# Performance work log

Measured on AMD Instinct MI355X. Metric: run time of the kernel, lower is better.

## Reference

```python
import jax, jax.numpy as jnp
import numpy as np

B, SEQ, H = 256, 200, 256
NFFT, HOP = 16, 8
FREQ = NFFT // 2 + 1          # 9
NSEG = SEQ // HOP + 1         # 26 (SEQ % HOP == 0 -> pad_len == 0)
FACTOR = 2


def _gelu(x):
    return jax.nn.gelu(x, approximate=False)  # torch nn.GELU / F.gelu default = exact erf


def _layernorm(x, w, b, eps=1e-12):
    u = x.mean(-1, keepdims=True)
    s = ((x - u) ** 2).mean(-1, keepdims=True)
    return w * (x - u) / jnp.sqrt(s + eps) + b


def _mixer(xr, xi, w1, b1, w2, b2):
    # complex MLP: einsum '...ijk,jkl->...ijl' with per-kept-dim weights
    e = lambda a, w: jnp.einsum('bijk,jkl->bijl', a, w)
    o1r = _gelu(e(xr, w1[0]) - e(xi, w1[1]) + b1[0])
    o1i = _gelu(e(xi, w1[0]) + e(xr, w1[1]) + b1[1])
    o2r = e(o1r, w2[0]) - e(o1i, w2[1]) + b2[0]
    # NOTE: faithful to the source bug: o1_image used in BOTH terms of o2_image
    o2i = e(o1i, w2[0]) + e(o1i, w2[1]) + b2[1]
    return o2r, o2i


def _stft(x):
    # torch.stft(n_fft=NFFT, hop=HOP, center=True, onesided=True, normalized=True,
    #            pad_mode='constant', window=None -> rectangular ones)
    pad = NFFT // 2
    xp = jnp.pad(x, ((0, 0), (pad, pad)))
    idx = jnp.arange(NSEG)[:, None] * HOP + jnp.arange(NFFT)[None, :]
    frames = xp[:, idx]                                    # [N, NSEG, NFFT]
    spec = jnp.fft.rfft(frames, axis=-1) * (NFFT ** -0.5)  # normalized=True
    return jnp.swapaxes(spec, -1, -2)                      # [N, FREQ, NSEG]


def _istft(spec):
    # torch.istft(center=True, normalized=True, rectangular window)
    n = spec.shape[0]
    frames = jnp.fft.irfft(jnp.swapaxes(spec, -1, -2) * (NFFT ** 0.5), n=NFFT, axis=-1)
    L = (NSEG - 1) * HOP + NFFT
    idx = (jnp.arange(NSEG)[:, None] * HOP + jnp.arange(NFFT)[None, :]).ravel()
    y = jnp.zeros((n, L), frames.dtype).at[:, idx].add(frames.reshape(n, -1))
    env = jnp.zeros((L,), frames.dtype).at[idx].add(1.0)   # window**2 overlap-add
    pad = NFFT // 2
    out_len = (NSEG - 1) * HOP                              # = SEQ
    return y[:, pad:pad + out_len] / env[pad:pad + out_len]


def setup_inputs() -> dict:
    key = jax.random.key(0)
    ks = jax.random.split(key, 24)
    p = lambda k, sh: jax.random.normal(k, sh, jnp.float32) * 0.02
    d = {}
    d["input_tensor"] = jax.random.normal(ks[0], (B, SEQ, H), jnp.float32)
    # grouped conv2d: weight [NSEG, 1, H, FREQ] -> stored as [NSEG, H, FREQ]
    d["conv_w"] = p(ks[1], (NSEG, H, FREQ)); d["conv_b"] = p(ks[2], (NSEG,))
    d["fm_w1"] = p(ks[3], (2, NSEG, FREQ, FREQ * FACTOR)); d["fm_b1"] = p(ks[4], (2, NSEG, FREQ * FACTOR))
    d["fm_w2"] = p(ks[5], (2, NSEG, FREQ * FACTOR, FREQ)); d["fm_b2"] = p(ks[6], (2, NSEG, FREQ))
    d["cm_w1"] = p(ks[7], (2, NSEG, H, H * FACTOR)); d["cm_b1"] = p(ks[8], (2, NSEG, H * FACTOR))
    d["cm_w2"] = p(ks[9], (2, NSEG, H * FACTOR, H)); d["cm_b2"] = p(ks[10], (2, NSEG, H))
    d["sm_w1"] = p(ks[11], (2, FREQ, NSEG, NSEG * FACTOR)); d["sm_b1"] = p(ks[12], (2, FREQ, NSEG * FACTOR))
    d["sm_w2"] = p(ks[13], (2, FREQ, NSEG * FACTOR, NSEG)); d["sm_b2"] = p(ks[14], (2, FREQ, NSEG))
    d["ln_w"] = jnp.ones((H,), jnp.float32); d["ln_b"] = jnp.zeros((H,), jnp.float32)
    d["ff_w1"] = p(ks[15], (H, 4 * H)); d["ff_b1"] = p(ks[16], (4 * H,))
    d["ff_w2"] = p(ks[17], (4 * H, H)); d["ff_b2"] = p(ks[18], (H,))
    d["ff_ln_w"] = jnp.ones((H,), jnp.float32); d["ff_ln_b"] = jnp.zeros((H,), jnp.float32)
    return d


def reference(input_tensor, conv_w, conv_b, fm_w1, fm_b1, fm_w2, fm_b2,
              cm_w1, cm_b1, cm_w2, cm_b2, sm_w1, sm_b1, sm_w2, sm_b2,
              ln_w, ln_b, ff_w1, ff_b1, ff_w2, ff_b2, ff_ln_w, ff_ln_b):
    b, seq, h = input_tensor.shape
    x = jnp.swapaxes(input_tensor, -1, -2).reshape(b * h, seq)  # pad_len == 0
    spec = _stft(x).reshape(b, h, FREQ, NSEG)
    xr, xi = spec.real, spec.imag
    xnorm = jnp.sqrt(xr ** 2 + xi ** 2)                         # [b,h,F,S]
    # grouped conv2d with full (H,FREQ) kernel == per-segment weighted sum
    w = jnp.einsum('bhfs,shf->bs', xnorm, conv_w) + conv_b
    w = w + jnp.exp(jnp.arange(1 - NSEG, 1, dtype=jnp.float32))  # exp decay bias
    xr = xr * w[:, None, None, :]
    xi = xi * w[:, None, None, :]
    # -> [b,h,S,F]: frequency mixing (kept=segment, mixed=freq)
    xr = jnp.swapaxes(xr, -1, -2); xi = jnp.swapaxes(xi, -1, -2)
    xr, xi = _mixer(xr, xi, fm_w1, fm_b1, fm_w2, fm_b2)
    # -> [b,F,S,h]: channel mixing (kept=segment, mixed=hidden)
    xr = jnp.swapaxes(xr, 1, 3); xi = jnp.swapaxes(xi, 1, 3)
    xr, xi = _mixer(xr, xi, cm_w1, cm_b1, cm_w2, cm_b2)
    # -> [b,h,F,S]: segment mixing (kept=freq, mixed=segment)
    xr = jnp.transpose(xr, (0, 3, 1, 2)); xi = jnp.transpose(xi, (0, 3, 1, 2))
    xr, xi = _mixer(xr, xi, sm_w1, sm_b1, sm_w2, sm_b2)
    spec = (xr + 1j * xi).reshape(b * h, FREQ, NSEG)
    y = _istft(spec)[:, :seq].reshape(b, h, seq)
    y = jnp.swapaxes(y, -1, -2)                                  # [b,seq,h]
    hs = _layernorm(y + input_tensor, ln_w, ln_b)                # dropout p=0
    ff = _gelu(hs @ ff_w1 + ff_b1) @ ff_w2 + ff_b2
    return _layernorm(ff + hs, ff_ln_w, ff_ln_b)
```

## Files before the change

kernel.cpp:

```cpp
#include <hip/hip_runtime.h>
#include <hip/hip_bf16.h>
#include <math.h>

typedef __hip_bfloat16 bf16;
typedef short bf16x8 __attribute__((ext_vector_type(8)));
typedef float f32x4 __attribute__((ext_vector_type(4)));

#define B_    256
#define SEQ_  200
#define H_    256
#define FREQ_ 9
#define NSEG_ 26
#define LDS64 64

__device__ __forceinline__ float ldb(const bf16* p, size_t i){ return __bfloat162float(p[i]); }
__device__ __forceinline__ void stb(bf16* p, size_t i, float v){ p[i] = __float2bfloat16(v); }
__device__ __forceinline__ short f2b(float v){ union{bf16 b; short s;} c; c.b = __float2bfloat16(v); return c.s; }
__device__ __forceinline__ unsigned short f2bu(float v){ union{bf16 b; unsigned short s;} c; c.b = __float2bfloat16(v); return c.s; }
__device__ __forceinline__ float gelu_(float x){
  float y  = 0.7978845608f*(x + 0.044715f*x*x*x);
  float ay = fabsf(y);
  float e  = __expf(-2.f*ay);
  float th = 1.f - 2.f*e*__builtin_amdgcn_rcpf(1.f + e);
  th = copysignf(th, y);
  return 0.5f*x*(1.f + th);
}

__device__ __constant__ float CT16[16] = {
  1.0f, 0.9238795325f, 0.7071067812f, 0.3826834324f, 0.0f, -0.3826834324f, -0.7071067812f, -0.9238795325f,
 -1.0f,-0.9238795325f,-0.7071067812f,-0.3826834324f, 0.0f,  0.3826834324f, 0.7071067812f,  0.9238795325f};
__device__ __constant__ float ST16[16] = {
  0.0f, 0.3826834324f, 0.7071067812f, 0.9238795325f, 1.0f,  0.9238795325f, 0.7071067812f,  0.3826834324f,
  0.0f,-0.3826834324f,-0.7071067812f,-0.9238795325f,-1.0f, -0.9238795325f,-0.7071067812f, -0.3826834324f};

__device__ __forceinline__ void gload16(const short* g, short* l){
  __builtin_amdgcn_global_load_lds(
      (const __attribute__((address_space(1))) unsigned int*)(const void*)g,
      (__attribute__((address_space(3))) unsigned int*)(void*)l, 16, 0, 0);
}

template<int ROWS>
__device__ __forceinline__ void stage_tile(short* lds, const short* src, int rstride, int tid){
  int rl = tid >> 3;
  int c  = tid & 7;
  #pragma unroll
  for(int p=0; p<ROWS/32; p++){
    int r = p*32 + rl;
    int csrc = c ^ (r & 7);
    gload16(src + (size_t)r*rstride + csrc*8, lds + r*LDS64 + c*8);
  }
}

__device__ __forceinline__ void mma_bk64(const short* lA, const short* lB, int wm, int wn,
                                         int lane, f32x4 acc[4][4]){
  int m_l = lane & 15, quad = lane >> 4;
  int sw = m_l & 7;
  #pragma unroll
  for(int ks=0; ks<64; ks+=32){
    int cs = (((ks>>3) + quad) ^ sw) * 8;
    bf16x8 a[4], b[4];
    #pragma unroll
    for(int i=0;i<4;i++) a[i] = *(const bf16x8*)&lA[(wm + i*16 + m_l)*LDS64 + cs];
    #pragma unroll
    for(int j=0;j<4;j++) b[j] = *(const bf16x8*)&lB[(wn + j*16 + m_l)*LDS64 + cs];
    #pragma unroll
    for(int i=0;i<4;i++)
      #pragma unroll
      for(int j=0;j<4;j++)
        acc[i][j] = __builtin_amdgcn_mfma_f32_16x16x32_bf16(a[i], b[j], acc[i][j], 0,0,0);
  }
}

__global__ __launch_bounds__(256) void k_prep_b1(const float* __restrict__ w1, short* __restrict__ B1t){
  int g = blockIdx.x;
  int jt = g & 7, ht = (g>>3)&3, p = (g>>5)&1, s = g>>6;
  __shared__ float tile[64][65];
  int t = threadIdx.x;
  const float* src = w1 + (size_t)p*3407872 + (size_t)s*131072;
  #pragma unroll
  for(int q=0;q<16;q++){
    int r = q*4 + (t>>6), c = t & 63;
    tile[r][c] = src[(size_t)(ht*64 + r)*512 + jt*64 + c];
  }
  __syncthreads();
  int n_l = t >> 2, kc = (t & 3)*16;
  short tA[16] __attribute__((aligned(16)));
  short tB[16] __attribute__((aligned(16)));
  #pragma unroll
  for(int i=0;i<16;i++){
    float v = tile[kc+i][n_l];
    tA[i] = (p==0) ? f2b(v) : f2b(-v);
    tB[i] = f2b(v);
  }
  int j = jt*64 + n_l, h = ht*64 + kc;
  size_t d1, d2;
  if(p==0){ d1 = ((size_t)(s*1024 + j))*512 + h;
            d2 = ((size_t)(s*1024 + 512 + j))*512 + 256 + h; }
  else    { d1 = ((size_t)(s*1024 + j))*512 + 256 + h;
            d2 = ((size_t)(s*1024 + 512 + j))*512 + h; }
  *(int4*)&B1t[d1] = *(int4*)&tA[0]; *(int4*)&B1t[d1+8] = *(int4*)&tA[8];
  *(int4*)&B1t[d2] = *(int4*)&tB[0]; *(int4*)&B1t[d2+8] = *(int4*)&tB[8];
}

__global__ __launch_bounds__(256) void k_prep_b2(const float* __restrict__ w2,
                                                 short* __restrict__ B2r, short* __restrict__ B2i){
  int g = blockIdx.x;
  int ht = g & 3, jt = (g>>2)&7, s = g>>5;
  __shared__ float t0[64][65], t1[64][65];
  int t = threadIdx.x;
  const float* s0 = w2 + (size_t)s*131072;
  const float* s1 = w2 + 3407872 + (size_t)s*131072;
  #pragma unroll
  for(int q=0;q<16;q++){
    int r = q*4 + (t>>6), c = t & 63;
    t0[r][c] = s0[(size_t)(jt*64 + r)*256 + ht*64 + c];
    t1[r][c] = s1[(size_t)(jt*64 + r)*256 + ht*64 + c];
  }
  __syncthreads();
  int n_l = t >> 2, jc = (t & 3)*16;
  short ta[16] __attribute__((aligned(16)));
  short tb[16] __attribute__((aligned(16)));
  short tc[16] __attribute__((aligned(16)));
  #pragma unroll
  for(int i=0;i<16;i++){
    float v0 = t0[jc+i][n_l], v1 = t1[jc+i][n_l];
    ta[i] = f2b(v0); tb[i] = f2b(-v1); tc[i] = f2b(v0+v1);
  }
  int n = ht*64 + n_l, j = jt*64 + jc;
  size_t dr = ((size_t)(s*256 + n))*1024 + j;
  size_t di = ((size_t)(s*256 + n))*512 + j;
  *(int4*)&B2r[dr]     = *(int4*)&ta[0]; *(int4*)&B2r[dr+8]     = *(int4*)&ta[8];
  *(int4*)&B2r[dr+512] = *(int4*)&tb[0]; *(int4*)&B2r[dr+520]   = *(int4*)&tb[8];
  *(int4*)&B2i[di]     = *(int4*)&tc[0]; *(int4*)&B2i[di+8]     = *(int4*)&tc[8];
}

__global__ __launch_bounds__(256) void k_transp(const float* __restrict__ src, short* __restrict__ dst,
                                                int R, int C){
  int ct = blockIdx.x % (C/64);
  int rt = blockIdx.x / (C/64);
  __shared__ float tile[64][65];
  int t = threadIdx.x;
  #pragma unroll
  for(int p=0;p<16;p++){
    int r = p*4 + (t>>6), c = t & 63;
    tile[r][c] = src[(size_t)(rt*64 + r)*C + ct*64 + c];
  }
  __syncthreads();
  int row_out = t >> 2, rc = (t & 3)*16;
  short tmp[16] __attribute__((aligned(16)));
  #pragma unroll
  for(int i=0;i<16;i++) tmp[i] = f2b(tile[rc+i][row_out]);
  size_t base = (size_t)(ct*64 + row_out)*R + rt*64 + rc;
  *(int4*)&dst[base] = *(int4*)&tmp[0]; *(int4*)&dst[base+8] = *(int4*)&tmp[8];
}

__global__ __launch_bounds__(256) void k_prep_sm(const float* __restrict__ w1, const float* __restrict__ w2,
                                                 short* __restrict__ B1sm, short* __restrict__ B2sm){
  int f = blockIdx.x;
  int t = threadIdx.x;
  for(int idx=t; idx<8192; idx+=256){
    int jp = idx >> 6, k = idx & 63;
    float v = 0.f;
    if(jp < 104){
      int j = (jp < 52) ? jp : jp - 52;
      if(k < 26){
        int s = k;
        v = (jp < 52) ? w1[f*1352 + s*52 + j] : w1[12168 + f*1352 + s*52 + j];
      } else if(k >= 32 && k < 58){
        int s = k - 32;
        v = (jp < 52) ? -w1[12168 + f*1352 + s*52 + j] : w1[f*1352 + s*52 + j];
      }
    }
    B1sm[(size_t)f*8192 + idx] = f2b(v);
  }
  for(int idx=t; idx<8192; idx+=256){
    int sop = idx >> 7, k = idx & 127;
    float v = 0.f;
    if(sop < 26){
      if(k < 52)       v = w2[f*1352 + k*26 + sop];
      else if(k < 104) v = -w2[12168 + f*1352 + (k-52)*26 + sop];
    } else if(sop < 52){
      int so = sop - 26;
      if(k >= 52 && k < 104)
        v = w2[f*1352 + (k-52)*26 + so] + w2[12168 + f*1352 + (k-52)*26 + so];
    }
    B2sm[(size_t)f*8192 + idx] = f2b(v);
  }
}

__global__ __launch_bounds__(256) void k_prep_fm(const float* __restrict__ w1, const float* __restrict__ w2,
                                                 short* __restrict__ B1fm, short* __restrict__ B2fm){
  int s = blockIdx.x;
  int t = threadIdx.x;
  for(int idx=t; idx<1536; idx+=256){
    int n = idx >> 5, k = idx & 31;
    float v = 0.f;
    if(n < 18){
      if(k < 9)       v = w1[s*162 + k*18 + n];
      else if(k < 18) v = -w1[4212 + s*162 + (k-9)*18 + n];
    } else if(n < 36){
      int j = n - 18;
      if(k < 9)       v = w1[4212 + s*162 + k*18 + j];
      else if(k < 18) v = w1[s*162 + (k-9)*18 + j];
    }
    B1fm[s*1536 + idx] = f2b(v);
  }
  for(int idx=t; idx<2048; idx+=256){
    int n = idx >> 6, k = idx & 63;
    float v = 0.f;
    if(n < 9){
      if(k < 18)      v = w2[s*162 + k*9 + n];
      else if(k < 36) v = -w2[4212 + s*162 + (k-18)*9 + n];
    } else if(n < 18){
      int f = n - 9;
      if(k >= 18 && k < 36)
        v = w2[s*162 + (k-18)*9 + f] + w2[4212 + s*162 + (k-18)*9 + f];
    }
    B2fm[s*2048 + idx] = f2b(v);
  }
}

__global__ __launch_bounds__(256) void k_prep_cw(const float* __restrict__ cw, float* __restrict__ cwT){
  int s = blockIdx.x; int t = threadIdx.x;
  __shared__ float tile[2304];
  for(int i=t; i<2304; i+=256) tile[i] = cw[s*2304 + i];
  __syncthreads();
  #pragma unroll
  for(int f=0; f<9; f++) cwT[(s*9+f)*256 + t] = tile[t*9+f];
}

#define LX1 40
#define LG1 72
__global__ __launch_bounds__(256) void k_sfm2(const float* __restrict__ inp,
                                              const float* __restrict__ cwT, const float* __restrict__ cb,
                                              const short* __restrict__ B1fm, const short* __restrict__ B2fm,
                                              const float* __restrict__ bb1, const float* __restrict__ bb2,
                                              bf16* __restrict__ oR, bf16* __restrict__ oI){
  int blk = blockIdx.x; int b = blk / NSEG_; int s = blk % NSEG_; int t = threadIdx.x;
  int lane = t & 63, wave = t >> 6, m_l = lane & 15, quad = lane >> 4;
  __shared__ __align__(16) short sm[20736];
  __shared__ float red[256];
  __shared__ float lb1f[48];
  short* lX  = sm;
  short* lB1 = sm + 10240;
  short* lG  = sm;
  short* lB2 = sm + 18432;

  {
    const short* src1 = B1fm + s*1536;
    for(int idx=t; idx<768; idx+=256){
      int r = idx >> 4, c = idx & 15;
      *(unsigned*)&lB1[r*LX1 + c*2] = *(const unsigned*)&src1[r*32 + c*2];
    }
    const short* src2 = B2fm + s*2048;
    for(int idx=t; idx<1024; idx+=256){
      int r = idx >> 5, c = idx & 31;
      *(unsigned*)&lB2[r*LG1 + c*2] = *(const unsigned*)&src2[r*64 + c*2];
    }
    if(t < 48) lb1f[t] = (t < 18) ? bb1[s*18 + t] : (t < 36 ? bb1[468 + s*18 + (t-18)] : 0.f);
  }

  float cwv[9];
  #pragma unroll
  for(int f=0;f<9;f++) cwv[f] = cwT[(s*9+f)*256 + t];

  float xv[16];
  int t0 = s*8 - 8;
  #pragma unroll
  for(int k=0;k<16;k++){
    int tt = t0 + k;
    xv[k] = (tt>=0 && tt<SEQ_) ? inp[(size_t)(b*SEQ_+tt)*H_ + t] : 0.0f;
  }
  float xr[9], xi[9];
  float acc = 0.f;
  #pragma unroll
  for(int f=0;f<FREQ_;f++){
    float ar=0.f, ai=0.f;
    #pragma unroll
    for(int k=0;k<16;k++){
      int m = (f*k) & 15;
      ar += xv[k]*CT16[m];
      ai -= xv[k]*ST16[m];
    }
    xr[f] = 0.25f*ar; xi[f] = 0.25f*ai;
    acc += sqrtf(xr[f]*xr[f] + xi[f]*xi[f]) * cwv[f];
  }

  red[t] = acc; __syncthreads();
  for(int off=128; off>0; off>>=1){ if(t<off) red[t] += red[t+off]; __syncthreads(); }
  float wv = red[0] + cb[s] + __expf((float)(s - (NSEG_-1)));

  {
    float vb[32];
    #pragma unroll
    for(int f=0;f<9;f++){ vb[f] = xr[f]*wv; vb[9+f] = xi[f]*wv; }
    #pragma unroll
    for(int k=18;k<32;k++) vb[k] = 0.f;
    union { unsigned u[16]; int4 v4[4]; } pk;
    #pragma unroll
    for(int c=0;c<16;c++)
      pk.u[c] = (unsigned)f2bu(vb[2*c]) | ((unsigned)f2bu(vb[2*c+1]) << 16);
    #pragma unroll
    for(int q=0;q<4;q++) *(int4*)&lX[t*LX1 + q*8] = pk.v4[q];
  }
  __syncthreads();

  int h0 = wave*64;
  f32x4 acc1[4][3];
  #pragma unroll
  for(int i=0;i<4;i++)
    #pragma unroll
    for(int j=0;j<3;j++) acc1[i][j] = (f32x4){0.f,0.f,0.f,0.f};
  {
    bf16x8 a1[4], b1v[3];
    #pragma unroll
    for(int i=0;i<4;i++) a1[i] = *(const bf16x8*)&lX[(h0 + i*16 + m_l)*LX1 + quad*8];
    #pragma unroll
    for(int j=0;j<3;j++) b1v[j] = *(const bf16x8*)&lB1[(j*16 + m_l)*LX1 + quad*8];
    #pragma unroll
    for(int i=0;i<4;i++)
      #pragma unroll
      for(int j=0;j<3;j++)
        acc1[i][j] = __builtin_amdgcn_mfma_f32_16x16x32_bf16(a1[i], b1v[j], acc1[i][j], 0,0,0);
  }
  __syncthreads();

  #pragma unroll
  for(int i=0;i<4;i++){
    #pragma unroll
    for(int j=0;j<3;j++){
      int n = j*16 + m_l;
      float bias = lb1f[n];
      #pragma unroll
      for(int r=0;r<4;r++){
        int row = h0 + i*16 + quad*4 + r;
        lG[row*LG1 + n] = f2b(gelu_(acc1[i][j][r] + bias));
      }
    }
  }
  #pragma unroll
  for(int c=0;c<8;c++) *(unsigned*)&lG[t*LG1 + 48 + c*2] = 0u;
  __syncthreads();

  f32x4 acc2[4][2];
  #pragma unroll
  for(int i=0;i<4;i++)
    #pragma unroll
    for(int j=0;j<2;j++) acc2[i][j] = (f32x4){0.f,0.f,0.f,0.f};
  #pragma unroll
  for(int ks=0; ks<64; ks+=32){
    bf16x8 a2[4], b2v[2];
    #pragma unroll
    for(int i=0;i<4;i++) a2[i] = *(const bf16x8*)&lG[(h0 + i*16 + m_l)*LG1 + ks + quad*8];
    #pragma unroll
    for(int j=0;j<2;j++) b2v[j] = *(const bf16x8*)&lB2[(j*16 + m_l)*LG1 + ks + quad*8];
    #pragma unroll
    for(int i=0;i<4;i++)
      #pragma unroll
      for(int j=0;j<2;j++)
        acc2[i][j] = __builtin_amdgcn_mfma_f32_16x16x32_bf16(a2[i], b2v[j], acc2[i][j], 0,0,0);
  }

  #pragma unroll
  for(int j=0;j<2;j++){
    int n = j*16 + m_l;
    if(n < 18){
      bool isI = n >= 9;
      int f = isI ? n-9 : n;
      float bias = isI ? bb2[234 + s*9 + f] : bb2[s*9 + f];
      bf16* outp = isI ? oI : oR;
      size_t base = ((size_t)(s*B_ + b)*FREQ_ + f)*H_;
      #pragma unroll
      for(int i=0;i<4;i++){
        int h = h0 + i*16 + quad*4;
        short pk[4] __attribute__((aligned(8)));
        #pragma unroll
        for(int r=0;r<4;r++) pk[r] = f2b(acc2[i][j][r] + bias);
        *(int2*)&outp[base + h] = *(const int2*)&pk[0];
      }
    }
  }
}

__global__ __launch_bounds__(256) void k_cm1(const bf16* __restrict__ Xr, const bf16* __restrict__ Xi,
                                             const short* __restrict__ B1t, const float* __restrict__ b1bias,
                                             short* __restrict__ H, int half){
  int nt = blockIdx.x & 7, mt = (blockIdx.x >> 3) % 9, s = blockIdx.x / 72;
  int tid = threadIdx.x, lane = tid & 63, wave = tid >> 6;
  int wm = (wave & 1)*64, wn = (wave >> 1)*64;
  __shared__ __align__(16) short lA[128*LDS64];
  __shared__ __align__(16) short lB[128*LDS64];
  f32x4 acc[4][4];
  #pragma unroll
  for(int i=0;i<4;i++)
    #pragma unroll
    for(int j=0;j<4;j++) acc[i][j] = (f32x4){0.f,0.f,0.f,0.f};
  int rowbase = half*1152 + mt*128;
  const short* Bbase = B1t + ((size_t)(s*1024 + nt*128))*512;
  for(int k0=0; k0<512; k0+=64){
    const short* Asrc = (k0 < 256)
      ? (const short*)(Xr + ((size_t)(s*2304 + rowbase))*256 + k0)
      : (const short*)(Xi + ((size_t)(s*2304 + rowbase))*256 + (k0-256));
    stage_tile<128>(lA, Asrc, 256, tid);
    stage_tile<128>(lB, Bbase + k0, 512, tid);
    __syncthreads();
    mma_bk64(lA, lB, wm, wn, lane, acc);
    __syncthreads();
  }
  int m_l = lane & 15, quad = lane >> 4;
  #pragma unroll
  for(int i=0;i<4;i++){
    #pragma unroll
    for(int j=0;j<4;j++){
      int n = nt*128 + wn + j*16 + m_l;
      float bias = (n < 512) ? b1bias[s*512 + n] : b1bias[13312 + s*512 + (n-512)];
      #pragma unroll
      for(int r=0;r<4;r++){
        int mrow = wm + i*16 + quad*4 + r;
        float v = gelu_(acc[i][j][r] + bias);
        H[((size_t)(s*1152 + mt*128 + mrow))*1024 + n] = f2b(v);
      }
    }
  }
}

__global__ __launch_bounds__(256) void k_cm2(const short* __restrict__ H,
                                             const short* __restrict__ B2r, const short* __restrict__ B2i,
                                             const float* __restrict__ b2bias,
                                             bf16* __restrict__ oR, bf16* __restrict__ oI, int half){
  int nt = blockIdx.x & 3, mt = (blockIdx.x>>2) % 9, s = blockIdx.x / 36;
  int tid = threadIdx.x, lane = tid & 63, wave = tid >> 6;
  int wm = (wave & 1)*64, wn = (wave >> 1)*64;
  bool isOi = nt >= 2;
  int n0 = (nt & 1)*128;
  int K = isOi ? 512 : 1024;
  int Aoff = isOi ? 512 : 0;
  int Bstride = isOi ? 512 : 1024;
  const short* Bb = isOi ? (B2i + ((size_t)(s*256 + n0))*512) : (B2r + ((size_t)(s*256 + n0))*1024);
  const short* Ab = H + ((size_t)(s*1152 + mt*128))*1024 + Aoff;
  __shared__ __align__(16) short lA[128*LDS64];
  __shared__ __align__(16) short lB[128*LDS64];
  f32x4 acc[4][4];
  #pragma unroll
  for(int i=0;i<4;i++)
    #pragma unroll
    for(int j=0;j<4;j++) acc[i][j] = (f32x4){0.f,0.f,0.f,0.f};
  for(int k0=0; k0<K; k0+=64){
    stage_tile<128>(lA, Ab + k0, 1024, tid);
    stage_tile<128>(lB, Bb + k0, Bstride, tid);
    __syncthreads();
    mma_bk64(lA, lB, wm, wn, lane, acc);
    __syncthreads();
  }
  int m_l = lane & 15, quad = lane >> 4;
  bf16* outp = isOi ? oI : oR;
  #pragma unroll
  for(int i=0;i<4;i++){
    #pragma unroll
    for(int j=0;j<4;j++){
      int n = n0 + wn + j*16 + m_l;
      float bias = b2bias[(isOi ? 6656 : 0) + s*256 + n];
      #pragma unroll
      for(int r=0;r<4;r++){
        int mrow = wm + i*16 + quad*4 + r;
        int rowg = half*1152 + mt*128 + mrow;
        stb(outp, ((size_t)rowg*NSEG_ + s)*256 + n, acc[i][j][r] + bias);
      }
    }
  }
}

#define LDX 72
#define LDG 136
__global__ __launch_bounds__(256) void k_smm(const bf16* __restrict__ iR, const bf16* __restrict__ iI,
                                             const short* __restrict__ B1sm, const short* __restrict__ B2sm,
                                             const float* __restrict__ bb1, const float* __restrict__ bb2,
                                             bf16* __restrict__ oR, bf16* __restrict__ oI){
  int blk = blockIdx.x;
  int f  = blk % 9;
  int hh = (blk/9) & 1;
  int bq = blk / 18;
  int t = threadIdx.x, lane = t & 63, wave = t >> 6;
  int m_l = lane & 15, quad = lane >> 4;
  __shared__ __align__(16) short sm[18432 + 8704];
  __shared__ float lb1[128];
  short* lX  = sm;
  short* lB1 = sm + 128*LDX;
  short* lG  = sm;
  short* lB2 = sm + 18432;
  int rbase = (bq*9 + f)*26;

  #pragma unroll
  for(int it=0; it<4; it++){
    int idx = it*256 + t;
    int r = idx >> 3, c = idx & 7;
    *(int4*)&lB1[r*LDX + c*8] = *(const int4*)&B1sm[(size_t)f*8192 + r*64 + c*8];
  }
  #pragma unroll
  for(int it=0; it<4; it++){
    int idx = it*256 + t;
    int r = idx >> 4, c = idx & 15;
    *(int4*)&lB2[r*LDG + c*8] = *(const int4*)&B2sm[(size_t)f*8192 + r*128 + c*8];
  }
  if(t < 128) lb1[t] = (t < 52) ? bb1[f*52 + t] : (t < 104 ? bb1[468 + f*52 + (t-52)] : 0.f);

  int hl = t & 127, g = t >> 7;
  #pragma unroll
  for(int it=0; it<13; it++){
    int a   = it*2 + g;
    int arr = a >= 13;
    int pr  = arr ? a-13 : a;
    int s0  = pr*2;
    const bf16* src = arr ? iI : iR;
    unsigned v0 = *(const unsigned short*)&src[((size_t)(rbase+s0  ))*256 + hh*128 + hl];
    unsigned v1 = *(const unsigned short*)&src[((size_t)(rbase+s0+1))*256 + hh*128 + hl];
    *(unsigned*)&lX[hl*LDX + arr*32 + s0] = v0 | (v1 << 16);
  }
  {
    int zb = g ? 58 : 26;
    #pragma unroll
    for(int i=0;i<3;i++) *(unsigned*)&lX[hl*LDX + zb + i*2] = 0u;
  }
  __syncthreads();

  int h0 = wave*32;
  f32x4 acc1[2][8];
  #pragma unroll
  for(int i=0;i<2;i++)
    #pragma unroll
    for(int j=0;j<8;j++) acc1[i][j] = (f32x4){0.f,0.f,0.f,0.f};
  #pragma unroll
  for(int ks=0; ks<64; ks+=32){
    bf16x8 av[2], bv[8];
    #pragma unroll
    for(int i=0;i<2;i++) av[i] = *(const bf16x8*)&lX[(h0 + i*16 + m_l)*LDX + ks + quad*8];
    #pragma unroll
    for(int j=0;j<8;j++) bv[j] = *(const bf16x8*)&lB1[(j*16 + m_l)*LDX + ks + quad*8];
    #pragma unroll
    for(int i=0;i<2;i++)
      #pragma unroll
      for(int j=0;j<8;j++)
        acc1[i][j] = __builtin_amdgcn_mfma_f32_16x16x32_bf16(av[i], bv[j], acc1[i][j], 0,0,0);
  }
  __syncthreads();

  #pragma unroll
  for(int i=0;i<2;i++){
    #pragma unroll
    for(int j=0;j<8;j++){
      int jp = j*16 + m_l;
      float bias = lb1[jp];
      #pragma unroll
      for(int r=0;r<4;r++){
        int hrow = h0 + i*16 + quad*4 + r;
        lG[hrow*LDG + jp] = f2b(gelu_(acc1[i][j][r] + bias));
      }
    }
  }
  __syncthreads();

  f32x4 acc2[2][4];
  #pragma unroll
  for(int i=0;i<2;i++)
    #pragma unroll
    for(int j=0;j<4;j++) acc2[i][j] = (f32x4){0.f,0.f,0.f,0.f};
  #pragma unroll
  for(int ks=0; ks<128; ks+=32){
    bf16x8 av[2], bv[4];
    #pragma unroll
    for(int i=0;i<2;i++) av[i] = *(const bf16x8*)&lG[(h0 + i*16 + m_l)*LDG + ks + quad*8];
    #pragma unroll
    for(int j=0;j<4;j++) bv[j] = *(const bf16x8*)&lB2[(j*16 + m_l)*LDG + ks + quad*8];
    #pragma unroll
    for(int i=0;i<2;i++)
      #pragma unroll
      for(int j=0;j<4;j++)
        acc2[i][j] = __builtin_amdgcn_mfma_f32_16x16x32_bf16(av[i], bv[j], acc2[i][j], 0,0,0);
  }

  #pragma unroll
  for(int j=0;j<4;j++){
    int sop = j*16 + m_l;
    if(sop < 52){
      int arr = sop >= 26;
      int so  = sop - (arr ? 26 : 0);
      float bias = bb2[(arr ? 234 : 0) + f*26 + so];
      bf16* outp = arr ? oI : oR;
      #pragma unroll
      for(int i=0;i<2;i++){
        int h = hh*128 + h0 + i*16 + quad*4;
        short pk[4] __attribute__((aligned(8)));
        #pragma unroll
        for(int r=0;r<4;r++) pk[r] = f2b(acc2[i][j][r] + bias);
        *(int2*)&outp[((size_t)(rbase + so))*256 + h] = *(const int2*)&pk[0];
      }
    }
  }
}

__global__ __launch_bounds__(256) void k_ist8(const bf16* __restrict__ iR, const bf16* __restrict__ iI,
                                              const float* __restrict__ inp,
                                              const float* __restrict__ lnw, const float* __restrict__ lnb,
                                              float* __restrict__ hs, bf16* __restrict__ hsb){
  int blk = blockIdx.x; int b = blk / 25; int o = blk % 25; int h = threadIdx.x;
  int lane = h & 63, wave = h >> 6;
  float rr[2][9], ii[2][8];
  #pragma unroll
  for(int p=0;p<2;p++){
    int s = o + p;
    size_t base = (size_t)b*FREQ_*NSEG_ + s;
    #pragma unroll
    for(int f=0;f<9;f++) rr[p][f] = ldb(iR, (base + f*NSEG_)*256 + h);
    #pragma unroll
    for(int f=1;f<8;f++) ii[p][f] = ldb(iI, (base + f*NSEG_)*256 + h);
  }
  float z[8];
  #pragma unroll
  for(int dt=0; dt<8; dt++){
    float v  = rr[0][0] + rr[1][0];
    float s8 = rr[0][8] + rr[1][8];
    v += (dt & 1) ? -s8 : s8;
    #pragma unroll
    for(int f=1;f<8;f++){
      int m1 = (f*(dt+8)) & 15;
      int m2 = (f*dt) & 15;
      v += 2.f*(rr[0][f]*CT16[m1] - ii[0][f]*ST16[m1]);
      v += 2.f*(rr[1][f]*CT16[m2] - ii[1][f]*ST16[m2]);
    }
    int t = o*8 + dt;
    z[dt] = 0.125f*v + inp[(size_t)(b*SEQ_+t)*H_ + h];
  }
  __shared__ float wsum[8][4], wsq[8][4];
  #pragma unroll
  for(int dt=0; dt<8; dt++){
    float sv = z[dt], sq = z[dt]*z[dt];
    #pragma unroll
    for(int msk=1; msk<64; msk<<=1){ sv += __shfl_xor(sv, msk); sq += __shfl_xor(sq, msk); }
    if(lane == 0){ wsum[dt][wave] = sv; wsq[dt][wave] = sq; }
  }
  __syncthreads();
  float gw = lnw[h], gb = lnb[h];
  #pragma unroll
  for(int dt=0; dt<8; dt++){
    float s1 = wsum[dt][0]+wsum[dt][1]+wsum[dt][2]+wsum[dt][3];
    float s2 = wsq[dt][0]+wsq[dt][1]+wsq[dt][2]+wsq[dt][3];
    float mean = s1*(1.f/256.f);
    float var  = s2*(1.f/256.f) - mean*mean;
    float inv  = rsqrtf(var + 1e-12f);
    float ov = gw*(z[dt]-mean)*inv + gb;
    int t = o*8 + dt;
    size_t oi = (size_t)(b*SEQ_+t)*H_ + h;
    hs[oi] = ov;
    stb(hsb, oi, ov);
  }
}

__global__ __launch_bounds__(256) void k_ff1m(const short* __restrict__ hsb, const short* __restrict__ fw1t,
                                              const float* __restrict__ fb1, short* __restrict__ hid, int row0){
  int nt = blockIdx.x & 7, mt = blockIdx.x >> 3;
  int tid = threadIdx.x, lane = tid & 63, wave = tid >> 6;
  int wm = (wave & 1)*64, wn = (wave >> 1)*64;
  __shared__ __align__(16) short lA[128*LDS64];
  __shared__ __align__(16) short lB[128*LDS64];
  f32x4 acc[4][4];
  #pragma unroll
  for(int i=0;i<4;i++)
    #pragma unroll
    for(int j=0;j<4;j++) acc[i][j] = (f32x4){0.f,0.f,0.f,0.f};
  const short* Ab = hsb + ((size_t)(row0 + mt*128))*256;
  const short* Bb = fw1t + ((size_t)(nt*128))*256;
  for(int k0=0; k0<256; k0+=64){
    stage_tile<128>(lA, Ab + k0, 256, tid);
    stage_tile<128>(lB, Bb + k0, 256, tid);
    __syncthreads();
    mma_bk64(lA, lB, wm, wn, lane, acc);
    __syncthreads();
  }
  int m_l = lane & 15, quad = lane >> 4;
  #pragma unroll
  for(int i=0;i<4;i++){
    #pragma unroll
    for(int j=0;j<4;j++){
      int n = nt*128 + wn + j*16 + m_l;
      float bias = fb1[n];
      #pragma unroll
      for(int r=0;r<4;r++){
        int mrow = wm + i*16 + quad*4 + r;
        hid[((size_t)(mt*128 + mrow))*1024 + n] = f2b(gelu_(acc[i][j][r] + bias));
      }
    }
  }
}

__global__ __launch_bounds__(256) void k_ff2m(const short* __restrict__ hid, const short* __restrict__ fw2t,
                                              const float* __restrict__ fb2, const float* __restrict__ hs,
                                              const float* __restrict__ lnw, const float* __restrict__ lnb,
                                              float* __restrict__ out, int row0){
  int mt = blockIdx.x;
  int tid = threadIdx.x, lane = tid & 63, wave = tid >> 6;
  int wn = wave*64;
  __shared__ __align__(16) short lA[64*LDS64];
  __shared__ __align__(16) short lB[256*LDS64];
  __shared__ float ssum[64][4], ssq[64][4];
  f32x4 acc[4][4];
  #pragma unroll
  for(int i=0;i<4;i++)
    #pragma unroll
    for(int j=0;j<4;j++) acc[i][j] = (f32x4){0.f,0.f,0.f,0.f};
  const short* Ab = hid + ((size_t)(mt*64))*1024;
  for(int k0=0; k0<1024; k0+=64){
    stage_tile<64>(lA, Ab + k0, 1024, tid);
    stage_tile<256>(lB, fw2t + k0, 1024, tid);
    __syncthreads();
    mma_bk64(lA, lB, 0, wn, lane, acc);
    __syncthreads();
  }
  int m_l = lane & 15, quad = lane >> 4;
  int rowg0 = row0 + mt*64;
  #pragma unroll
  for(int i=0;i<4;i++){
    #pragma unroll
    for(int j=0;j<4;j++){
      int col = wn + j*16 + m_l;
      float bias = fb2[col];
      #pragma unroll
      for(int r=0;r<4;r++){
        int mrow = i*16 + quad*4 + r;
        acc[i][j][r] += bias + hs[(size_t)(rowg0+mrow)*256 + col];
      }
    }
  }
  #pragma unroll
  for(int i=0;i<4;i++){
    #pragma unroll
    for(int r=0;r<4;r++){
      float sv = 0.f, sq = 0.f;
      #pragma unroll
      for(int j=0;j<4;j++){ float v = acc[i][j][r]; sv += v; sq += v*v; }
      #pragma unroll
      for(int msk=1; msk<16; msk<<=1){ sv += __shfl_xor(sv, msk); sq += __shfl_xor(sq, msk); }
      if(m_l == 0){ int mrow = i*16 + quad*4 + r; ssum[mrow][wave] = sv; ssq[mrow][wave] = sq; }
    }
  }
  __syncthreads();
  if(tid < 64){
    float s1 = ssum[tid][0]+ssum[tid][1]+ssum[tid][2]+ssum[tid][3];
    float s2 = ssq[tid][0]+ssq[tid][1]+ssq[tid][2]+ssq[tid][3];
    float mean = s1*(1.f/256.f);
    float var  = s2*(1.f/256.f) - mean*mean;
    ssum[tid][0] = mean;
    ssq[tid][0]  = rsqrtf(var + 1e-12f);
  }
  __syncthreads();
  #pragma unroll
  for(int i=0;i<4;i++){
    #pragma unroll
    for(int j=0;j<4;j++){
      int col = wn + j*16 + m_l;
      float gw = lnw[col], gb = lnb[col];
      #pragma unroll
      for(int r=0;r<4;r++){
        int mrow = i*16 + quad*4 + r;
        float mean = ssum[mrow][0], inv = ssq[mrow][0];
        out[(size_t)(rowg0+mrow)*256 + col] = (acc[i][j][r] - mean)*inv*gw + gb;
      }
    }
  }
}

extern "C" void kernel_launch(void* const* d_in, const int* in_sizes, int n_in,
                              void* d_out, int out_size, void* d_ws, size_t ws_size,
                              hipStream_t stream){
  const float* inp    = (const float*)d_in[0];
  const float* conv_w = (const float*)d_in[1];
  const float* conv_b = (const float*)d_in[2];
  const float* fm_w1  = (const float*)d_in[3];
  const float* fm_b1  = (const float*)d_in[4];
  const float* fm_w2  = (const float*)d_in[5];
  const float* fm_b2  = (const float*)d_in[6];
  const float* cm_w1  = (const float*)d_in[7];
  const float* cm_b1  = (const float*)d_in[8];
  const float* cm_w2  = (const float*)d_in[9];
  const float* cm_b2  = (const float*)d_in[10];
  const float* sm_w1  = (const float*)d_in[11];
  const float* sm_b1  = (const float*)d_in[12];
  const float* sm_w2  = (const float*)d_in[13];
  const float* sm_b2  = (const float*)d_in[14];
  const float* ln_w   = (const float*)d_in[15];
  const float* ln_b   = (const float*)d_in[16];
  const float* ff_w1  = (const float*)d_in[17];
  const float* ff_b1  = (const float*)d_in[18];
  const float* ff_w2  = (const float*)d_in[19];
  const float* ff_b2  = (const float*)d_in[20];
  const float* ffln_w = (const float*)d_in[21];
  const float* ffln_b = (const float*)d_in[22];
  float* out = (float*)d_out;

  const size_t NS = (size_t)B_ * NSEG_ * FREQ_ * H_;
  const size_t HN = (size_t)NSEG_ * 1152 * 1024;
  short* ws = (short*)d_ws;
  bf16*  b0   = (bf16*)ws;
  bf16*  b1   = (bf16*)(ws + NS);
  bf16*  b2   = (bf16*)(ws + 2*NS);
  bf16*  b3   = (bf16*)(ws + 3*NS);
  short* H    = ws + 4*NS;
  short* B1t  = H + HN;
  short* B2r  = B1t + (size_t)26*1024*512;
  short* B2i  = B2r + (size_t)26*256*1024;
  short* fw1t = B2i + (size_t)26*256*512;
  short* fw2t = fw1t + 262144;
  short* B1sm = fw2t + 262144;
  short* B2sm = B1sm + 73728;
  short* B1fm = B2sm + 73728;
  short* B2fm = B1fm + 39936;
  float* cwT  = (float*)(B2fm + 53248);
  float* hs   = (float*)b0;
  bf16*  hsb  = (bf16*)H;
  short* hid  = (short*)b2;

  k_prep_b1<<<1664, 256, 0, stream>>>(cm_w1, B1t);
  k_prep_b2<<<832,  256, 0, stream>>>(cm_w2, B2r, B2i);
  k_transp <<<64,   256, 0, stream>>>(ff_w1, fw1t, 256, 1024);
  k_transp <<<64,   256, 0, stream>>>(ff_w2, fw2t, 1024, 256);
  k_prep_sm<<<9,    256, 0, stream>>>(sm_w1, sm_w2, B1sm, B2sm);
  k_prep_fm<<<26,   256, 0, stream>>>(fm_w1, fm_w2, B1fm, B2fm);
  k_prep_cw<<<26,   256, 0, stream>>>(conv_w, cwT);

  k_sfm2<<<B_*NSEG_, 256, 0, stream>>>(inp, cwT, conv_b, B1fm, B2fm, fm_b1, fm_b2, b2, b3);
  for(int half=0; half<2; half++){
    k_cm1<<<26*72, 256, 0, stream>>>(b2, b3, B1t, cm_b1, H, half);
    k_cm2<<<26*36, 256, 0, stream>>>(H, B2r, B2i, cm_b2, b0, b1, half);
  }
  k_smm<<<B_*2*FREQ_, 256, 0, stream>>>(b0, b1, B1sm, B2sm, sm_b1, sm_b2, b2, b3);
  k_ist8<<<B_*25, 256, 0, stream>>>(b2, b3, inp, ln_w, ln_b, hs, hsb);
  for(int c=0; c<2; c++){
    int row0 = c*25600;
    k_ff1m<<<1600, 256, 0, stream>>>((const short*)hsb, fw1t, ff_b1, hid, row0);
    k_ff2m<<<400,  256, 0, stream>>>(hid, fw2t, ff_b2, hs, ffln_w, ffln_b, out, row0);
  }
}
```

Baseline: 840.3 us.

## Compute STFT via MFMA DFT matrix and fold segment weight post-GEMM

The per-thread scalar 16-point DFT in the STFT/frequency-mixing kernel is replaced by a bf16 MFMA GEMM against a DFT matrix built in LDS. The 256-thread tree reduction is replaced by wave shuffles plus a four-entry LDS sum. The segment weight is now applied to the first mixer GEMM output instead of its input. This cuts VALU work and barrier count but quantises the raw input and the spectrum to bf16, which may reduce accuracy.

```diff
diff --git a/kernel.cpp b/kernel.cpp
--- a/kernel.cpp
+++ b/kernel.cpp
@@ -17,6 +17,7 @@
 __device__ __forceinline__ void stb(bf16* p, size_t i, float v){ p[i] = __float2bfloat16(v); }
 __device__ __forceinline__ short f2b(float v){ union{bf16 b; short s;} c; c.b = __float2bfloat16(v); return c.s; }
 __device__ __forceinline__ unsigned short f2bu(float v){ union{bf16 b; unsigned short s;} c; c.b = __float2bfloat16(v); return c.s; }
+__device__ __forceinline__ float b2f(unsigned short u){ union{unsigned short s; bf16 b;} c; c.s = u; return __bfloat162float(c.b); }
 __device__ __forceinline__ float gelu_(float x){
   float y  = 0.7978845608f*(x + 0.044715f*x*x*x);
   float ay = fabsf(y);
@@ -231,7 +232,7 @@
 
 #define LX1 40
 #define LG1 72
-__global__ __launch_bounds__(256) void k_sfm2(const float* __restrict__ inp,
+__global__ __launch_bounds__(256) void k_sfm3(const float* __restrict__ inp,
                                               const float* __restrict__ cwT, const float* __restrict__ cb,
                                               const short* __restrict__ B1fm, const short* __restrict__ B2fm,
                                               const float* __restrict__ bb1, const float* __restrict__ bb2,
@@ -239,12 +240,14 @@
   int blk = blockIdx.x; int b = blk / NSEG_; int s = blk % NSEG_; int t = threadIdx.x;
   int lane = t & 63, wave = t >> 6, m_l = lane & 15, quad = lane >> 4;
   __shared__ __align__(16) short sm[20736];
-  __shared__ float red[256];
   __shared__ float lb1f[48];
-  short* lX  = sm;
-  short* lB1 = sm + 10240;
-  short* lG  = sm;
-  short* lB2 = sm + 18432;
+  __shared__ float wred[4];
+  short* lFt  = sm;
+  short* lX   = sm;
+  short* lB1  = sm + 10240;
+  short* lDft = sm + 12160;
+  short* lG   = sm;
+  short* lB2  = sm + 18432;
 
   {
     const short* src1 = B1fm + s*1536;
@@ -258,59 +261,90 @@
       *(unsigned*)&lB2[r*LG1 + c*2] = *(const unsigned*)&src2[r*64 + c*2];
     }
     if(t < 48) lb1f[t] = (t < 18) ? bb1[s*18 + t] : (t < 36 ? bb1[468 + s*18 + (t-18)] : 0.f);
-  }
-
+    #pragma unroll
+    for(int q=0;q<4;q++){
+      int idx = q*256 + t;
+      int n = idx >> 5, k = idx & 31;
+      float v = 0.f;
+      if(k < 16){
+        if(n < 9)       v =  0.25f*CT16[(n*k) & 15];
+        else if(n < 18) v = -0.25f*ST16[((n-9)*k) & 15];
+      }
+      lDft[n*LX1 + k] = f2b(v);
+    }
+  }
   float cwv[9];
   #pragma unroll
   for(int f=0;f<9;f++) cwv[f] = cwT[(s*9+f)*256 + t];
-
-  float xv[16];
-  int t0 = s*8 - 8;
-  #pragma unroll
-  for(int k=0;k<16;k++){
-    int tt = t0 + k;
-    xv[k] = (tt>=0 && tt<SEQ_) ? inp[(size_t)(b*SEQ_+tt)*H_ + t] : 0.0f;
-  }
-  float xr[9], xi[9];
-  float acc = 0.f;
-  #pragma unroll
-  for(int f=0;f<FREQ_;f++){
-    float ar=0.f, ai=0.f;
-    #pragma unroll
-    for(int k=0;k<16;k++){
-      int m = (f*k) & 15;
-      ar += xv[k]*CT16[m];
-      ai -= xv[k]*ST16[m];
-    }
-    xr[f] = 0.25f*ar; xi[f] = 0.25f*ai;
-    acc += sqrtf(xr[f]*xr[f] + xi[f]*xi[f]) * cwv[f];
-  }
-
-  red[t] = acc; __syncthreads();
-  for(int off=128; off>0; off>>=1){ if(t<off) red[t] += red[t+off]; __syncthreads(); }
-  float wv = red[0] + cb[s] + __expf((float)(s - (NSEG_-1)));
-
   {
-    float vb[32];
-    #pragma unroll
-    for(int f=0;f<9;f++){ vb[f] = xr[f]*wv; vb[9+f] = xi[f]*wv; }
-    #pragma unroll
-    for(int k=18;k<32;k++) vb[k] = 0.f;
-    union { unsigned u[16]; int4 v4[4]; } pk;
-    #pragma unroll
-    for(int c=0;c<16;c++)
-      pk.u[c] = (unsigned)f2bu(vb[2*c]) | ((unsigned)f2bu(vb[2*c+1]) << 16);
-    #pragma unroll
-    for(int q=0;q<4;q++) *(int4*)&lX[t*LX1 + q*8] = pk.v4[q];
+    int t0 = s*8 - 8;
+    unsigned pk[8];
+    #pragma unroll
+    for(int c=0;c<8;c++){
+      int t1 = t0 + 2*c, t2 = t0 + 2*c + 1;
+      float v1 = (t1>=0 && t1<SEQ_) ? inp[(size_t)(b*SEQ_+t1)*H_ + t] : 0.0f;
+      float v2 = (t2>=0 && t2<SEQ_) ? inp[(size_t)(b*SEQ_+t2)*H_ + t] : 0.0f;
+      pk[c] = (unsigned)f2bu(v1) | ((unsigned)f2bu(v2) << 16);
+    }
+    *(int4*)&lFt[t*LX1 + 0] = *(const int4*)&pk[0];
+    *(int4*)&lFt[t*LX1 + 8] = *(const int4*)&pk[4];
+    int4 z = {0,0,0,0};
+    *(int4*)&lFt[t*LX1 + 16] = z;
+    *(int4*)&lFt[t*LX1 + 24] = z;
   }
   __syncthreads();
 
   int h0 = wave*64;
+  f32x4 accD[4][2];
+  {
+    bf16x8 a[4], bD[2];
+    #pragma unroll
+    for(int i=0;i<4;i++) a[i] = *(const bf16x8*)&lFt[(h0 + i*16 + m_l)*LX1 + quad*8];
+    #pragma unroll
+    for(int j=0;j<2;j++) bD[j] = *(const bf16x8*)&lDft[(j*16 + m_l)*LX1 + quad*8];
+    #pragma unroll
+    for(int i=0;i<4;i++)
+      #pragma unroll
+      for(int j=0;j<2;j++)
+        accD[i][j] = __builtin_amdgcn_mfma_f32_16x16x32_bf16(a[i], bD[j], (f32x4){0.f,0.f,0.f,0.f}, 0,0,0);
+  }
+  __syncthreads();
+
+  #pragma unroll
+  for(int i=0;i<4;i++)
+    #pragma unroll
+    for(int j=0;j<2;j++){
+      int n = j*16 + m_l;
+      #pragma unroll
+      for(int r=0;r<4;r++){
+        int h = h0 + i*16 + quad*4 + r;
+        lX[h*LX1 + n] = f2b(accD[i][j][r]);
+      }
+    }
+  __syncthreads();
+
+  float g = 0.f;
+  {
+    unsigned u[10];
+    *(int4*)&u[0] = *(const int4*)&lX[t*LX1 + 0];
+    *(int4*)&u[4] = *(const int4*)&lX[t*LX1 + 8];
+    *(int2*)&u[8] = *(const int2*)&lX[t*LX1 + 16];
+    float xv[18];
+    #pragma unroll
+    for(int c=0;c<9;c++){ xv[2*c] = b2f((unsigned short)(u[c]&0xFFFF)); xv[2*c+1] = b2f((unsigned short)(u[c]>>16)); }
+    #pragma unroll
+    for(int f=0;f<9;f++){
+      float xr = xv[f], xi = xv[9+f];
+      g += sqrtf(xr*xr + xi*xi) * cwv[f];
+    }
+    #pragma unroll
+    for(int msk=1; msk<64; msk<<=1) g += __shfl_xor(g, msk);
+    if(lane == 0) wred[wave] = g;
+  }
+  __syncthreads();
+  float wv = wred[0]+wred[1]+wred[2]+wred[3] + cb[s] + __expf((float)(s - (NSEG_-1)));
+
   f32x4 acc1[4][3];
-  #pragma unroll
-  for(int i=0;i<4;i++)
-    #pragma unroll
-    for(int j=0;j<3;j++) acc1[i][j] = (f32x4){0.f,0.f,0.f,0.f};
   {
     bf16x8 a1[4], b1v[3];
     #pragma unroll
@@ -321,7 +355,7 @@
     for(int i=0;i<4;i++)
       #pragma unroll
       for(int j=0;j<3;j++)
-        acc1[i][j] = __builtin_amdgcn_mfma_f32_16x16x32_bf16(a1[i], b1v[j], acc1[i][j], 0,0,0);
+        acc1[i][j] = __builtin_amdgcn_mfma_f32_16x16x32_bf16(a1[i], b1v[j], (f32x4){0.f,0.f,0.f,0.f}, 0,0,0);
   }
   __syncthreads();
 
@@ -334,7 +368,7 @@
       #pragma unroll
       for(int r=0;r<4;r++){
         int row = h0 + i*16 + quad*4 + r;
-        lG[row*LG1 + n] = f2b(gelu_(acc1[i][j][r] + bias));
+        lG[row*LG1 + n] = f2b(gelu_(acc1[i][j][r]*wv + bias));
       }
     }
   }
@@ -826,7 +860,7 @@
   k_prep_fm<<<26,   256, 0, stream>>>(fm_w1, fm_w2, B1fm, B2fm);
   k_prep_cw<<<26,   256, 0, stream>>>(conv_w, cwT);
 
-  k_sfm2<<<B_*NSEG_, 256, 0, stream>>>(inp, cwT, conv_b, B1fm, B2fm, fm_b1, fm_b2, b2, b3);
+  k_sfm3<<<B_*NSEG_, 256, 0, stream>>>(inp, cwT, conv_b, B1fm, B2fm, fm_b1, fm_b2, b2, b3);
   for(int half=0; half<2; half++){
     k_cm1<<<26*72, 256, 0, stream>>>(b2, b3, B1t, cm_b1, H, half);
     k_cm2<<<26*36, 256, 0, stream>>>(H, B2r, B2i, cm_b2, b0, b1, half);
```

After: 895.1 us. 6.5% more time.
